# Kernel optimization log

Hardware: AMD Instinct MI355X
Metric: run time of the kernel (lower is better)

Reference implementation:

```python
import jax, jax.numpy as jnp
import numpy as np

NOPEN = 64
NNIN = 16
NUM_OUTPUT = 64
NLAYER = 4
H = 0.1
TF = 1.0
N_NODES = 50000
N_EDGES = 1600000


def setup_inputs() -> dict:
    key = jax.random.key(0)
    k1, k2, k3, k4, k5, k6 = jax.random.split(key, 6)
    xn = jax.random.normal(k1, (1, NNIN, N_NODES), dtype=jnp.float32)
    iInd = jax.random.randint(k2, (N_EDGES,), 0, N_NODES)
    jInd = jax.random.randint(k3, (N_EDGES,), 0, N_NODES)
    # learned parameters per original init
    K1Nopen = jax.random.normal(k4, (NOPEN, NNIN), dtype=jnp.float32) * 0.01
    KN1 = jnp.eye(NOPEN, dtype=jnp.float32) + jax.random.uniform(k5, (NOPEN, NOPEN), dtype=jnp.float32) * 0.001
    KNclose = jax.random.normal(k6, (NUM_OUTPUT, NOPEN), dtype=jnp.float32) * 0.01
    return {"xn": xn, "iInd": iInd, "jInd": jInd, "n_nodes": N_NODES,
            "K1Nopen": K1Nopen, "KN1": KN1, "KNclose": KNclose}


def _gcn_norm(I, J, n_nodes, dtype):
    # add self-loops, symmetric normalization deg^{-1/2}[row]*deg^{-1/2}[col]
    loops = jnp.arange(n_nodes, dtype=I.dtype)
    I2 = jnp.concatenate([I, loops])
    J2 = jnp.concatenate([J, loops])
    ew = jnp.ones(I2.shape[0], dtype=dtype)
    deg = jax.ops.segment_sum(ew, J2, num_segments=n_nodes)
    dinv = jnp.where(deg > 0, 1.0 / jnp.sqrt(deg), 0.0)
    w = dinv[I2] * dinv[J2]
    return I2, J2, w


def reference(xn, iInd, jInd, n_nodes, K1Nopen, KN1, KNclose):
    I, J, w = _gcn_norm(iInd, jInd, n_nodes, xn.dtype)  # [E+N]

    # OpenFlatLayer: 1x1 conv1d with K1Nopen + relu (openclose=True, norm=False)
    x = jax.nn.relu(jnp.einsum('oi,bin->bon', K1Nopen, xn))  # [1, nopen, N]

    dt = TF / NLAYER
    wb = w[None, None, :]
    for _ in range(NLAYER):
        # nodeGrad: edge features [1, nopen, E]
        g = wb * (x[:, :, I] - x[:, :, J])
        # singleLayer (openclose=False): conv(K), relu, conv(K.t())
        z = jax.nn.relu(jnp.einsum('oi,bie->boe', KN1, g))
        z = jnp.einsum('io,bie->boe', KN1, z)
        # edgeDiv: scatter-add w*z at I minus at J
        wz = jnp.moveaxis(wb * z, -1, 0)  # [E, 1, nopen]
        div = (jax.ops.segment_sum(wz, I, num_segments=n_nodes)
               - jax.ops.segment_sum(wz, J, num_segments=n_nodes))
        div = jnp.moveaxis(div, 0, -1)  # [1, nopen, N]
        # forward Euler: step layer returns -h*div, integrated with dt
        x = x - dt * H * div

    # CloseLayer: 1x1 conv1d, squeeze().t(), log_softmax over channels
    xc = jnp.einsum('oi,bin->bon', KNclose, x)[0].T  # [N, num_output]
    return jax.nn.log_softmax(xc, axis=1)
```

## Files before the change

### kernel.cpp

```cpp
#include <hip/hip_runtime.h>

#define NN 50000
#define NE 1600000
#define C 64
#define NIN 16
#define DTH 0.025f
#define ASC 16.0f
#define USC 64.0f
#define SDIV 16384.0f
#define SLOT 128

#define NB2 256
#define NPB 196
#define CAP 16384
#define ABLK 1024
#define EPB 1563
#define RND 2048
#define BINC 32
#define GSTR 16

typedef _Float16 f16x2 __attribute__((ext_vector_type(2)));
typedef float f32x2 __attribute__((ext_vector_type(2)));
union U32H2 { uint32_t u; f16x2 h; };

#define RL(x, l) __int_as_float(__builtin_amdgcn_readlane(__float_as_int(x), (l)))

__global__ void k_setup(const float* __restrict__ KN1, const float* __restrict__ KNc,
                        float* __restrict__ M2s, float* __restrict__ KMs,
                        int* __restrict__ gcur) {
    if (threadIdx.x < NB2) gcur[threadIdx.x * GSTR] = 0;
    for (int idx = threadIdx.x; idx < C * C; idx += blockDim.x) {
        int p = idx >> 6, o = idx & 63;
        float s1 = 0.f, s2 = 0.f;
        for (int i = 0; i < C; i++) {
            s1 = fmaf(KN1[o * C + i], KN1[p * C + i], s1);
            s2 = fmaf(KNc[o * C + i], KN1[p * C + i], s2);
        }
        M2s[idx] = s1;
        KMs[idx] = s2;
    }
}

static __device__ __forceinline__ void store_u8(uint32_t* __restrict__ u8, int n, int lane, float su) {
    float v1 = __shfl_down(su, 1, 64);
    float v2 = __shfl_down(su, 2, 64);
    float v3 = __shfl_down(su, 3, 64);
    if ((lane & 3) == 0) {
        int p0 = __builtin_amdgcn_cvt_pk_fp8_f32(su, v1, 0, false);
        int p1 = __builtin_amdgcn_cvt_pk_fp8_f32(v2, v3, p0, true);
        u8[n * 16 + (lane >> 2)] = (uint32_t)p1;
    }
}

__launch_bounds__(512)
__global__ void k_binA_open(const int* __restrict__ iInd, const int* __restrict__ jInd,
                            int* __restrict__ gcur, uint32_t* __restrict__ stg,
                            const float* __restrict__ xn, const float* __restrict__ K1,
                            const float* __restrict__ KN1, const float* __restrict__ KNc,
                            _Float16* __restrict__ u0, uint32_t* __restrict__ u8,
                            float* __restrict__ co) {
    __shared__ __align__(16) char smem[36864];
    __shared__ int bcnt[NB2];
    __shared__ int gbase[NB2];
    __shared__ float sxn[NIN][17];
    uint32_t (*bins)[BINC] = (uint32_t(*)[BINC])smem;
    int tid = threadIdx.x;
    int eBeg = blockIdx.x * EPB;
    int eEnd = eBeg + EPB; if (eEnd > NE) eEnd = NE;
    for (int rb = eBeg; rb < eEnd; rb += RND) {
        for (int b = tid; b < NB2; b += 512) bcnt[b] = 0;
        __syncthreads();
        int rEnd = rb + RND; if (rEnd > eEnd) rEnd = eEnd;
        for (int e = rb + tid; e < rEnd; e += 512) {
            int i = __builtin_nontemporal_load(&iInd[e]);
            int j = __builtin_nontemporal_load(&jInd[e]);
            {
                int b = (unsigned)i / NPB;
                uint32_t ent = ((unsigned)(i - b * NPB) << 17) | (unsigned)j;
                int pos = atomicAdd(&bcnt[b], 1);
                if (pos < BINC) bins[b][pos] = ent;
                else { int gp = atomicAdd(&gcur[b * GSTR], 1);
                       if (gp < CAP) stg[(size_t)b * CAP + gp] = ent; }
            }
            {
                int b = (unsigned)j / NPB;
                uint32_t ent = ((unsigned)(j - b * NPB) << 17) | 0x10000u | (unsigned)i;
                int pos = atomicAdd(&bcnt[b], 1);
                if (pos < BINC) bins[b][pos] = ent;
                else { int gp = atomicAdd(&gcur[b * GSTR], 1);
                       if (gp < CAP) stg[(size_t)b * CAP + gp] = ent; }
            }
        }
        __syncthreads();
        if (tid < NB2) {
            int c = bcnt[tid]; if (c > BINC) c = BINC;
            gbase[tid] = (c > 0) ? atomicAdd(&gcur[tid * GSTR], c) : 0;
        }
        __syncthreads();
        for (int idx = tid; idx < NB2 * BINC; idx += 512) {
            int b = idx >> 5, k = idx & (BINC - 1);
            int c = bcnt[b]; if (c > BINC) c = BINC;
            if (k < c) {
                int pos = gbase[b] + k;
                if (pos < CAP) stg[(size_t)b * CAP + pos] = bins[b][k];
            }
        }
        __syncthreads();
    }
    float* sK1 = (float*)smem;
    float* sU  = sK1 + NIN * C;
    float* sC  = sU + C * C;
    for (int idx = tid; idx < NIN * C; idx += 512) {
        int i = idx >> 6, o = idx & 63;
        sK1[idx] = K1[o * NIN + i];
    }
    for (int idx = tid; idx < C * C; idx += 512) {
        int o = idx >> 6, p = idx & 63;
        int sw = (o << 6) | (p ^ ((o & 7) << 2));
        sU[sw] = KN1[idx];
        sC[sw] = KNc[idx];
    }
    int wv = tid >> 6, lane = tid & 63;
    int mb = lane << 6, lx = (lane & 7) << 2;
    int w2 = wv * 2;
    int nit = 3 + (blockIdx.x < 53 ? 1 : 0);
    int fi = tid >> 4, ft = tid & 15;
    float vpre = 0.f;
    if (tid < 256) vpre = xn[fi * NN + blockIdx.x * 16 + ft];
    for (int it = 0; it < nit; it++) {
        __syncthreads();
        if (tid < 256) sxn[fi][ft] = vpre;
        __syncthreads();
        if (it + 1 < nit && tid < 256)
            vpre = xn[fi * NN + blockIdx.x * 16 + (it + 1) * 16384 + ft];
        int pr = blockIdx.x * 8 + wv + it * 8192;
        int nA = pr * 2, nB = nA + 1;
        float xA = 0.f, xB = 0.f;
#pragma unroll
        for (int i = 0; i < NIN; i++) {
            float k1 = sK1[i * C + lane];
            xA = fmaf(k1, sxn[i][w2], xA);
            xB = fmaf(k1, sxn[i][w2 + 1], xB);
        }
        xA = fmaxf(xA, 0.f); xB = fmaxf(xB, 0.f);
        float uA0 = 0.f, uA1 = 0.f, uB0 = 0.f, uB1 = 0.f;
        float cA0 = 0.f, cA1 = 0.f, cB0 = 0.f, cB1 = 0.f;
#pragma unroll
        for (int p0 = 0; p0 < C; p0 += 4) {
            const float4 mu = *(const float4*)&sU[mb + (p0 ^ lx)];
            const float4 mc = *(const float4*)&sC[mb + (p0 ^ lx)];
            float a0 = RL(xA, p0 + 0), a1 = RL(xA, p0 + 1);
            float a2 = RL(xA, p0 + 2), a3 = RL(xA, p0 + 3);
            float b0 = RL(xB, p0 + 0), b1 = RL(xB, p0 + 1);
            float b2 = RL(xB, p0 + 2), b3 = RL(xB, p0 + 3);
            uA0 = fmaf(mu.x, a0, uA0); uA1 = fmaf(mu.y, a1, uA1);
            uA0 = fmaf(mu.z, a2, uA0); uA1 = fmaf(mu.w, a3, uA1);
            uB0 = fmaf(mu.x, b0, uB0); uB1 = fmaf(mu.y, b1, uB1);
            uB0 = fmaf(mu.z, b2, uB0); uB1 = fmaf(mu.w, b3, uB1);
            cA0 = fmaf(mc.x, a0, cA0); cA1 = fmaf(mc.y, a1, cA1);
            cA0 = fmaf(mc.z, a2, cA0); cA1 = fmaf(mc.w, a3, cA1);
            cB0 = fmaf(mc.x, b0, cB0); cB1 = fmaf(mc.y, b1, cB1);
            cB0 = fmaf(mc.z, b2, cB0); cB1 = fmaf(mc.w, b3, cB1);
        }
        float uA = uA0 + uA1, uB = uB0 + uB1;
        u0[(size_t)nA * C + lane] = (_Float16)uA;
        u0[(size_t)nB * C + lane] = (_Float16)uB;
        store_u8(u8, nA, lane, uA * USC);
        store_u8(u8, nB, lane, uB * USC);
        co[(size_t)nA * C + lane] = cA0 + cA1;
        co[(size_t)nB * C + lane] = cB0 + cB1;
    }
}

#define LADJ (NPB * SLOT)
__launch_bounds__(1024)
__global__ void k_binB(const int* __restrict__ gcur, const uint32_t* __restrict__ stg,
                       unsigned* __restrict__ pk, float* __restrict__ dinv,
                       uint32_t* __restrict__ adjp) {
    __shared__ unsigned lcnt[NPB];
    __shared__ uint32_t ladj[LADJ];
    int b = blockIdx.x, tid = threadIdx.x;
    if (tid < NPB) lcnt[tid] = 0;
    __syncthreads();
    int cnt = gcur[b * GSTR]; if (cnt > CAP) cnt = CAP;
    int n0 = b * NPB;
    for (int k = tid; k < cnt; k += 1024) {
        uint32_t ent = stg[(size_t)b * CAP + k];
        int tl = (int)(ent >> 17);
        unsigned sign = (ent >> 16) & 1u;
        unsigned other = ent & 0xFFFFu;
        unsigned ret = atomicAdd(&lcnt[tl], 1u + (sign << 16));
        unsigned slot = ret & 0xFFFFu;
        if (slot < SLOT) ladj[(tl << 7) + slot] = other | (sign << 31);
    }
    __syncthreads();
    if (tid < NPB) {
        int n = n0 + tid;
        if (n < NN) {
            unsigned v = lcnt[tid];
            unsigned c = v & 0xFFFFu; if (c > SLOT) c = SLOT;
            unsigned deg = (v >> 16) + 1u;
            pk[n] = (deg << 16) | c;
            dinv[n] = 1.0f / sqrtf((float)deg);
        }
    }
    int nval = NN - n0; if (nval > NPB) nval = NPB; if (nval < 0) nval = 0;
    int totv = (nval << 7) >> 2;
    uint4* gdst = (uint4*)(adjp + ((size_t)n0 << 7));
    const uint4* lsrc = (const uint4*)ladj;
    for (int v = tid; v < totv; v += 1024) gdst[v] = lsrc[v];
}

__global__ void k_weight(const unsigned* __restrict__ pk, const float* __restrict__ dinv,
                         uint32_t* __restrict__ adjp) {
    int idx = blockIdx.x * 256 + threadIdx.x;
    int n = idx >> 7, p = idx & (SLOT - 1);
    int cnt = (int)(pk[n] & 0xFFFFu); if (cnt > SLOT) cnt = SLOT;
    int pad = (cnt + 31) & ~31;
    if (p < cnt) {
        uint32_t e = adjp[idx];
        int other = (int)(e & 0xFFFFu);
        float a = ASC * dinv[n] * dinv[other];
        if (e >> 31) a = -a;
        U32H2 t; t.u = (unsigned)other; t.h.y = (_Float16)a;
        adjp[idx] = t.u;
    } else if (p < pad) {
        adjp[idx] = 0u;
    }
}

#define ACCR(WW, QQ, A01, A23, U01, U23) {                                    \
    U32H2 aw; aw.u = (WW);                                                    \
    float a_ = (float)aw.h.y;                                                 \
    f32x2 av_; av_.x = a_; av_.y = a_;                                        \
    f32x2 lo_ = __builtin_amdgcn_cvt_pk_f32_fp8((int)(QQ), false);            \
    f32x2 hi_ = __builtin_amdgcn_cvt_pk_f32_fp8((int)(QQ), true);             \
    f32x2 t01_ = av_ * ((U01) - lo_);                                         \
    f32x2 t23_ = av_ * ((U23) - hi_);                                         \
    t01_ = __builtin_elementwise_max(t01_, zz);                               \
    t23_ = __builtin_elementwise_max(t23_, zz);                               \
    A01 = av_ * t01_ + A01;                                                   \
    A23 = av_ * t23_ + A23;                                                   \
}

#define GATHER2_BODY(PKA, ADJP, U8R)                                          \
    uint32_t unqA = (U8R)[nA * 16 + li];                                      \
    uint32_t unqB = (U8R)[nB * 16 + li];                                      \
    f32x2 uA01 = __builtin_amdgcn_cvt_pk_f32_fp8((int)unqA, false);           \
    f32x2 uA23 = __builtin_amdgcn_cvt_pk_f32_fp8((int)unqA, true);            \
    f32x2 uB01 = __builtin_amdgcn_cvt_pk_f32_fp8((int)unqB, false);           \
    f32x2 uB23 = __builtin_amdgcn_cvt_pk_f32_fp8((int)unqB, true);            \
    uint2 pk2_ = *(const uint2*)&(PKA)[nA];                                   \
    int degA = (int)(pk2_.x & 0xFFFFu); if (degA > SLOT) degA = SLOT;         \
    int degB = (int)(pk2_.y & 0xFFFFu); if (degB > SLOT) degB = SLOT;         \
    int padA = (degA + 31) & ~31, padB = (degB + 31) & ~31;                   \
    int baseA = nA << 7, baseB = nB << 7;                                     \
    int maxPad = padA > padB ? padA : padB;                                   \
    f32x2 zz; zz.x = 0.f; zz.y = 0.f;                                         \
    f32x2 aA01 = zz, aA23 = zz, aB01 = zz, aB23 = zz;                         \
    uint32_t wA[8], wB[8];                                                    \
    if (padA > 0) {                                                           \
        _Pragma("unroll")                                                     \
        for (int r = 0; r < 8; r++) wA[r] = (ADJP)[baseA + r * 4 + g];        \
    }                                                                         \
    if (padB > 0) {                                                           \
        _Pragma("unroll")                                                     \
        for (int r = 0; r < 8; r++) wB[r] = (ADJP)[baseB + r * 4 + g];        \
    }                                                                         \
    for (int c0 = 0; c0 < maxPad; c0 += 32) {                                 \
        uint32_t qA[8], qB[8], wA2[8], wB2[8];                                \
        bool dA = c0 < padA, dB = c0 < padB;                                  \
        bool dA2 = c0 + 32 < padA, dB2 = c0 + 32 < padB;                      \
        if (dA) {                                                             \
            _Pragma("unroll")                                                 \
            for (int r = 0; r < 8; r++) qA[r] = (U8R)[(wA[r] & 0xFFFFu) * 16 + li]; \
        }                                                                     \
        if (dB) {                                                             \
            _Pragma("unroll")                                                 \
            for (int r = 0; r < 8; r++) qB[r] = (U8R)[(wB[r] & 0xFFFFu) * 16 + li]; \
        }                                                                     \
        if (dA2) {                                                            \
            _Pragma("unroll")                                                 \
            for (int r = 0; r < 8; r++) wA2[r] = (ADJP)[baseA + c0 + 32 + r * 4 + g]; \
        }                                                                     \
        if (dB2) {                                                            \
            _Pragma("unroll")                                                 \
            for (int r = 0; r < 8; r++) wB2[r] = (ADJP)[baseB + c0 + 32 + r * 4 + g]; \
        }                                                                     \
        if (dA) {                                                             \
            _Pragma("unroll")                                                 \
            for (int r = 0; r < 8; r++) ACCR(wA[r], qA[r], aA01, aA23, uA01, uA23) \
        }                                                                     \
        if (dB) {                                                             \
            _Pragma("unroll")                                                 \
            for (int r = 0; r < 8; r++) ACCR(wB[r], qB[r], aB01, aB23, uB01, uB23) \
        }                                                                     \
        if (dA2) {                                                            \
            _Pragma("unroll")                                                 \
            for (int r = 0; r < 8; r++) wA[r] = wA2[r];                       \
        }                                                                     \
        if (dB2) {                                                            \
            _Pragma("unroll")                                                 \
            for (int r = 0; r < 8; r++) wB[r] = wB2[r];                       \
        }                                                                     \
    }                                                                         \
    float aA0 = aA01.x, aA1 = aA01.y, aA2 = aA23.x, aA3 = aA23.y;             \
    float aB0 = aB01.x, aB1 = aB01.y, aB2 = aB23.x, aB3 = aB23.y;             \
    aA0 += __shfl_xor(aA0, 16, 64); aA0 += __shfl_xor(aA0, 32, 64);           \
    aA1 += __shfl_xor(aA1, 16, 64); aA1 += __shfl_xor(aA1, 32, 64);           \
    aA2 += __shfl_xor(aA2, 16, 64); aA2 += __shfl_xor(aA2, 32, 64);           \
    aA3 += __shfl_xor(aA3, 16, 64); aA3 += __shfl_xor(aA3, 32, 64);           \
    aB0 += __shfl_xor(aB0, 16, 64); aB0 += __shfl_xor(aB0, 32, 64);           \
    aB1 += __shfl_xor(aB1, 16, 64); aB1 += __shfl_xor(aB1, 32, 64);           \
    aB2 += __shfl_xor(aB2, 16, 64); aB2 += __shfl_xor(aB2, 32, 64);           \
    aB3 += __shfl_xor(aB3, 16, 64); aB3 += __shfl_xor(aB3, 32, 64);           \
    float rA0 = __shfl(aA0, lane >> 2, 64), rA1 = __shfl(aA1, lane >> 2, 64); \
    float rA2 = __shfl(aA2, lane >> 2, 64), rA3 = __shfl(aA3, lane >> 2, 64); \
    float rB0 = __shfl(aB0, lane >> 2, 64), rB1 = __shfl(aB1, lane >> 2, 64); \
    float rB2 = __shfl(aB2, lane >> 2, 64), rB3 = __shfl(aB3, lane >> 2, 64); \
    float sA_lane = (lane & 2) ? ((lane & 1) ? rA3 : rA2)                     \
                               : ((lane & 1) ? rA1 : rA0);                    \
    float sB_lane = (lane & 2) ? ((lane & 1) ? rB3 : rB2)                     \
                               : ((lane & 1) ? rB1 : rB0);

#define STAGE_MT(SMT, SRC) {                                                  \
    for (int idx = threadIdx.x; idx < C * C; idx += 256) {                    \
        int p_ = idx >> 6, c_ = idx & 63;                                     \
        (SMT)[(c_ << 6) | (p_ ^ ((c_ & 7) << 2))] = (SRC)[idx];               \
    }                                                                         \
}

#define MATVEC2(SMT, SAV, SBV, DUA, DUB) {                                    \
    float mA0_ = 0.f, mA1_ = 0.f, mB0_ = 0.f, mB1_ = 0.f;                     \
    int mb_ = (lane << 6), lx_ = (lane & 7) << 2;                             \
    _Pragma("unroll")                                                         \
    for (int p0 = 0; p0 < 64; p0 += 4) {                                      \
        const float4 mv = *(const float4*)&(SMT)[mb_ + (p0 ^ lx_)];           \
        mA0_ = fmaf(mv.x, RL(SAV, p0 + 0), mA0_);                             \
        mA1_ = fmaf(mv.y, RL(SAV, p0 + 1), mA1_);                             \
        mA0_ = fmaf(mv.z, RL(SAV, p0 + 2), mA0_);                             \
        mA1_ = fmaf(mv.w, RL(SAV, p0 + 3), mA1_);                             \
        mB0_ = fmaf(mv.x, RL(SBV, p0 + 0), mB0_);                             \
        mB1_ = fmaf(mv.y, RL(SBV, p0 + 1), mB1_);                             \
        mB0_ = fmaf(mv.z, RL(SBV, p0 + 2), mB0_);                             \
        mB1_ = fmaf(mv.w, RL(SBV, p0 + 3), mB1_);                             \
    }                                                                         \
    DUA = mA0_ + mA1_; DUB = mB0_ + mB1_;                                     \
}

__launch_bounds__(256, 6)
__global__ void k_gather_upd(const unsigned* __restrict__ pk, const uint32_t* __restrict__ adjp,
                             const uint32_t* __restrict__ u8r, const _Float16* __restrict__ ucur,
                             const float* __restrict__ M2s, float* __restrict__ sacc,
                             _Float16* __restrict__ unext, uint32_t* __restrict__ u8w, int beta) {
    __shared__ float sMt[C * C];
    STAGE_MT(sMt, M2s)
    __syncthreads();
    int wv = threadIdx.x >> 6, lane = threadIdx.x & 63;
    int g = lane >> 4, li = lane & 15;
    int nA = (blockIdx.x * 4 + wv) * 2;
    int nB = nA + 1;
    GATHER2_BODY(pk, adjp, u8r)
    float duA, duB;
    MATVEC2(sMt, sA_lane, sB_lane, duA, duB)
    float unewA = (float)ucur[(size_t)nA * C + lane] - (DTH / SDIV) * duA;
    float unewB = (float)ucur[(size_t)nB * C + lane] - (DTH / SDIV) * duB;
    unext[(size_t)nA * C + lane] = (_Float16)unewA;
    unext[(size_t)nB * C + lane] = (_Float16)unewB;
    store_u8(u8w, nA, lane, unewA * USC);
    store_u8(u8w, nB, lane, unewB * USC);
    size_t ixA = (size_t)nA * C + lane, ixB = (size_t)nB * C + lane;
    sacc[ixA] = beta ? (sacc[ixA] + sA_lane) : sA_lane;
    sacc[ixB] = beta ? (sacc[ixB] + sB_lane) : sB_lane;
}

__launch_bounds__(256, 6)
__global__ void k_gather_close(const unsigned* __restrict__ pk, const uint32_t* __restrict__ adjp,
                               const uint32_t* __restrict__ u8r, const float* __restrict__ KMs,
                               const float* __restrict__ sacc, const float* __restrict__ co,
                               float* __restrict__ out) {
    __shared__ float sKMt[C * C];
    STAGE_MT(sKMt, KMs)
    __syncthreads();
    int wv = threadIdx.x >> 6, lane = threadIdx.x & 63;
    int g = lane >> 4, li = lane & 15;
    int nA = (blockIdx.x * 4 + wv) * 2;
    int nB = nA + 1;
    GATHER2_BODY(pk, adjp, u8r)
    float stotA = sA_lane + sacc[(size_t)nA * C + lane];
    float stotB = sB_lane + sacc[(size_t)nB * C + lane];
    float dxA, dxB;
    MATVEC2(sKMt, stotA, stotB, dxA, dxB)
    float oA = co[(size_t)nA * C + lane] - (DTH / SDIV) * dxA;
    float oB = co[(size_t)nB * C + lane] - (DTH / SDIV) * dxB;
    float mA = oA, mB = oB;
#pragma unroll
    for (int off2 = 32; off2; off2 >>= 1) {
        mA = fmaxf(mA, __shfl_xor(mA, off2, 64));
        mB = fmaxf(mB, __shfl_xor(mB, off2, 64));
    }
    float sumA = expf(oA - mA), sumB = expf(oB - mB);
#pragma unroll
    for (int off2 = 32; off2; off2 >>= 1) {
        sumA += __shfl_xor(sumA, off2, 64);
        sumB += __shfl_xor(sumB, off2, 64);
    }
    out[(size_t)nA * C + lane] = oA - mA - logf(sumA);
    out[(size_t)nB * C + lane] = oB - mB - logf(sumB);
}

extern "C" void kernel_launch(void* const* d_in, const int* in_sizes, int n_in,
                              void* d_out, int out_size, void* d_ws, size_t ws_size,
                              hipStream_t stream) {
    (void)in_sizes; (void)n_in; (void)out_size; (void)ws_size;
    const float* xn   = (const float*)d_in[0];
    const int* iInd   = (const int*)d_in[1];
    const int* jInd   = (const int*)d_in[2];
    const float* K1   = (const float*)d_in[4];
    const float* KN1  = (const float*)d_in[5];
    const float* KNc  = (const float*)d_in[6];
    float* out = (float*)d_out;

    char* base = (char*)d_ws;
    size_t off = 0;
    auto alloc = [&](size_t bytes) { char* p = base + off; off = (off + bytes + 255) & ~(size_t)255; return p; };
    float* M2s  = (float*)alloc(C * C * 4);
    float* KMs  = (float*)alloc(C * C * 4);
    int* gcur   = (int*)alloc(NB2 * GSTR * 4);
    unsigned* pk = (unsigned*)alloc(NN * 4);
    float* dinv = (float*)alloc(NN * 4);
    float* co   = (float*)alloc((size_t)NN * C * 4);
    float* sacc = (float*)alloc((size_t)NN * C * 4);
    _Float16* ua = (_Float16*)alloc((size_t)NN * C * 2);
    _Float16* ub = (_Float16*)alloc((size_t)NN * C * 2);
    uint32_t* u8a = (uint32_t*)alloc((size_t)NN * 16 * 4);
    uint32_t* u8b = (uint32_t*)alloc((size_t)NN * 16 * 4);
    uint32_t* stg = (uint32_t*)alloc((size_t)NB2 * CAP * 4);
    uint32_t* adjp = (uint32_t*)alloc((size_t)NN * SLOT * 4);

    k_setup<<<1, 256, 0, stream>>>(KN1, KNc, M2s, KMs, gcur);
    k_binA_open<<<ABLK, 512, 0, stream>>>(iInd, jInd, gcur, stg, xn, K1, KN1, KNc, ua, u8a, co);
    k_binB<<<NB2, 1024, 0, stream>>>(gcur, stg, pk, dinv, adjp);
    k_weight<<<(NN * SLOT) / 256, 256, 0, stream>>>(pk, dinv, adjp);

    const int GB = NN / 8;
    k_gather_upd<<<GB, 256, 0, stream>>>(pk, adjp, u8a, ua, M2s, sacc, ub, u8b, 0);
    k_gather_upd<<<GB, 256, 0, stream>>>(pk, adjp, u8b, ub, M2s, sacc, ua, u8a, 1);
    k_gather_upd<<<GB, 256, 0, stream>>>(pk, adjp, u8a, ua, M2s, sacc, ub, u8b, 1);
    k_gather_close<<<GB, 256, 0, stream>>>(pk, adjp, u8b, KMs, sacc, co, out);
}
```

Measured before the change: 460.7 us.

## Vectorize edge weighting, drop adjacency prefetch, use persistent gather grid

The edge-weight kernel now handles four adjacency slots per thread with 128-bit loads and stores, using a quarter of the threads. The gather loop no longer double-buffers the next chunk of adjacency words, which frees registers, and the launch bounds rise from 6 to 8 waves per SIMD. The gather and close kernels become grid-stride loops over a fixed 2048-block grid, so the 64x64 matrix is staged into shared memory once per block instead of once per 8 nodes. In exchange, adjacency loads are no longer overlapped with the feature gathers, which can expose more memory latency.

```diff
diff --git a/kernel.cpp b/kernel.cpp
--- a/kernel.cpp
+++ b/kernel.cpp
@@ -18,6 +18,7 @@
 #define RND 2048
 #define BINC 32
 #define GSTR 16
+#define GGRID 2048
 
 typedef _Float16 f16x2 __attribute__((ext_vector_type(2)));
 typedef float f32x2 __attribute__((ext_vector_type(2)));
@@ -211,22 +212,36 @@
     for (int v = tid; v < totv; v += 1024) gdst[v] = lsrc[v];
 }
 
+__launch_bounds__(256)
 __global__ void k_weight(const unsigned* __restrict__ pk, const float* __restrict__ dinv,
                          uint32_t* __restrict__ adjp) {
     int idx = blockIdx.x * 256 + threadIdx.x;
-    int n = idx >> 7, p = idx & (SLOT - 1);
+    int n = idx >> 5, p4 = (idx & 31) << 2;
     int cnt = (int)(pk[n] & 0xFFFFu); if (cnt > SLOT) cnt = SLOT;
     int pad = (cnt + 31) & ~31;
-    if (p < cnt) {
-        uint32_t e = adjp[idx];
-        int other = (int)(e & 0xFFFFu);
-        float a = ASC * dinv[n] * dinv[other];
-        if (e >> 31) a = -a;
-        U32H2 t; t.u = (unsigned)other; t.h.y = (_Float16)a;
-        adjp[idx] = t.u;
-    } else if (p < pad) {
-        adjp[idx] = 0u;
-    }
+    if (p4 >= pad) return;
+    size_t base = ((size_t)n << 7) + p4;
+    uint4 e = *(const uint4*)&adjp[base];
+    float dn = ASC * dinv[n];
+    uint4 o;
+    {
+        uint32_t r[4] = {e.x, e.y, e.z, e.w};
+        uint32_t w[4];
+#pragma unroll
+        for (int k = 0; k < 4; k++) {
+            if (p4 + k < cnt) {
+                int other = (int)(r[k] & 0xFFFFu);
+                float a = dn * dinv[other];
+                if (r[k] >> 31) a = -a;
+                U32H2 t; t.u = (unsigned)other; t.h.y = (_Float16)a;
+                w[k] = t.u;
+            } else {
+                w[k] = 0u;
+            }
+        }
+        o.x = w[0]; o.y = w[1]; o.z = w[2]; o.w = w[3];
+    }
+    *(uint4*)&adjp[base] = o;
 }
 
 #define ACCR(WW, QQ, A01, A23, U01, U23) {                                    \
@@ -258,35 +273,25 @@
     int maxPad = padA > padB ? padA : padB;                                   \
     f32x2 zz; zz.x = 0.f; zz.y = 0.f;                                         \
     f32x2 aA01 = zz, aA23 = zz, aB01 = zz, aB23 = zz;                         \
-    uint32_t wA[8], wB[8];                                                    \
-    if (padA > 0) {                                                           \
-        _Pragma("unroll")                                                     \
-        for (int r = 0; r < 8; r++) wA[r] = (ADJP)[baseA + r * 4 + g];        \
-    }                                                                         \
-    if (padB > 0) {                                                           \
-        _Pragma("unroll")                                                     \
-        for (int r = 0; r < 8; r++) wB[r] = (ADJP)[baseB + r * 4 + g];        \
-    }                                                                         \
     for (int c0 = 0; c0 < maxPad; c0 += 32) {                                 \
-        uint32_t qA[8], qB[8], wA2[8], wB2[8];                                \
+        uint32_t wA[8], qA[8], wB[8], qB[8];                                  \
         bool dA = c0 < padA, dB = c0 < padB;                                  \
-        bool dA2 = c0 + 32 < padA, dB2 = c0 + 32 < padB;                      \
         if (dA) {                                                             \
             _Pragma("unroll")                                                 \
+            for (int r = 0; r < 8; r++) wA[r] = (ADJP)[baseA + c0 + r * 4 + g]; \
+        }                                                                     \
+        if (dB) {                                                             \
+            _Pragma("unroll")                                                 \
+            for (int r = 0; r < 8; r++) wB[r] = (ADJP)[baseB + c0 + r * 4 + g]; \
+        }                                                                     \
+        if (dA) {                                                             \
+            _Pragma("unroll")                                                 \
             for (int r = 0; r < 8; r++) qA[r] = (U8R)[(wA[r] & 0xFFFFu) * 16 + li]; \
         }                                                                     \
         if (dB) {                                                             \
             _Pragma("unroll")                                                 \
             for (int r = 0; r < 8; r++) qB[r] = (U8R)[(wB[r] & 0xFFFFu) * 16 + li]; \
         }                                                                     \
-        if (dA2) {                                                            \
-            _Pragma("unroll")                                                 \
-            for (int r = 0; r < 8; r++) wA2[r] = (ADJP)[baseA + c0 + 32 + r * 4 + g]; \
-        }                                                                     \
-        if (dB2) {                                                            \
-            _Pragma("unroll")                                                 \
-            for (int r = 0; r < 8; r++) wB2[r] = (ADJP)[baseB + c0 + 32 + r * 4 + g]; \
-        }                                                                     \
         if (dA) {                                                             \
             _Pragma("unroll")                                                 \
             for (int r = 0; r < 8; r++) ACCR(wA[r], qA[r], aA01, aA23, uA01, uA23) \
@@ -294,14 +299,6 @@
         if (dB) {                                                             \
             _Pragma("unroll")                                                 \
             for (int r = 0; r < 8; r++) ACCR(wB[r], qB[r], aB01, aB23, uB01, uB23) \
-        }                                                                     \
-        if (dA2) {                                                            \
-            _Pragma("unroll")                                                 \
-            for (int r = 0; r < 8; r++) wA[r] = wA2[r];                       \
-        }                                                                     \
-        if (dB2) {                                                            \
-            _Pragma("unroll")                                                 \
-            for (int r = 0; r < 8; r++) wB[r] = wB2[r];                       \
         }                                                                     \
     }                                                                         \
     float aA0 = aA01.x, aA1 = aA01.y, aA2 = aA23.x, aA3 = aA23.y;             \
@@ -348,7 +345,7 @@
     DUA = mA0_ + mA1_; DUB = mB0_ + mB1_;                                     \
 }
 
-__launch_bounds__(256, 6)
+__launch_bounds__(256, 8)
 __global__ void k_gather_upd(const unsigned* __restrict__ pk, const uint32_t* __restrict__ adjp,
                              const uint32_t* __restrict__ u8r, const _Float16* __restrict__ ucur,
                              const float* __restrict__ M2s, float* __restrict__ sacc,
@@ -358,23 +355,25 @@
     __syncthreads();
     int wv = threadIdx.x >> 6, lane = threadIdx.x & 63;
     int g = lane >> 4, li = lane & 15;
-    int nA = (blockIdx.x * 4 + wv) * 2;
-    int nB = nA + 1;
-    GATHER2_BODY(pk, adjp, u8r)
-    float duA, duB;
-    MATVEC2(sMt, sA_lane, sB_lane, duA, duB)
-    float unewA = (float)ucur[(size_t)nA * C + lane] - (DTH / SDIV) * duA;
-    float unewB = (float)ucur[(size_t)nB * C + lane] - (DTH / SDIV) * duB;
-    unext[(size_t)nA * C + lane] = (_Float16)unewA;
-    unext[(size_t)nB * C + lane] = (_Float16)unewB;
-    store_u8(u8w, nA, lane, unewA * USC);
-    store_u8(u8w, nB, lane, unewB * USC);
-    size_t ixA = (size_t)nA * C + lane, ixB = (size_t)nB * C + lane;
-    sacc[ixA] = beta ? (sacc[ixA] + sA_lane) : sA_lane;
-    sacc[ixB] = beta ? (sacc[ixB] + sB_lane) : sB_lane;
-}
-
-__launch_bounds__(256, 6)
+    for (int grp = blockIdx.x; grp < NN / 8; grp += GGRID) {
+        int nA = (grp * 4 + wv) * 2;
+        int nB = nA + 1;
+        GATHER2_BODY(pk, adjp, u8r)
+        float duA, duB;
+        MATVEC2(sMt, sA_lane, sB_lane, duA, duB)
+        float unewA = (float)ucur[(size_t)nA * C + lane] - (DTH / SDIV) * duA;
+        float unewB = (float)ucur[(size_t)nB * C + lane] - (DTH / SDIV) * duB;
+        unext[(size_t)nA * C + lane] = (_Float16)unewA;
+        unext[(size_t)nB * C + lane] = (_Float16)unewB;
+        store_u8(u8w, nA, lane, unewA * USC);
+        store_u8(u8w, nB, lane, unewB * USC);
+        size_t ixA = (size_t)nA * C + lane, ixB = (size_t)nB * C + lane;
+        sacc[ixA] = beta ? (sacc[ixA] + sA_lane) : sA_lane;
+        sacc[ixB] = beta ? (sacc[ixB] + sB_lane) : sB_lane;
+    }
+}
+
+__launch_bounds__(256, 8)
 __global__ void k_gather_close(const unsigned* __restrict__ pk, const uint32_t* __restrict__ adjp,
                                const uint32_t* __restrict__ u8r, const float* __restrict__ KMs,
                                const float* __restrict__ sacc, const float* __restrict__ co,
@@ -384,29 +383,31 @@
     __syncthreads();
     int wv = threadIdx.x >> 6, lane = threadIdx.x & 63;
     int g = lane >> 4, li = lane & 15;
-    int nA = (blockIdx.x * 4 + wv) * 2;
-    int nB = nA + 1;
-    GATHER2_BODY(pk, adjp, u8r)
-    float stotA = sA_lane + sacc[(size_t)nA * C + lane];
-    float stotB = sB_lane + sacc[(size_t)nB * C + lane];
-    float dxA, dxB;
-    MATVEC2(sKMt, stotA, stotB, dxA, dxB)
-    float oA = co[(size_t)nA * C + lane] - (DTH / SDIV) * dxA;
-    float oB = co[(size_t)nB * C + lane] - (DTH / SDIV) * dxB;
-    float mA = oA, mB = oB;
+    for (int grp = blockIdx.x; grp < NN / 8; grp += GGRID) {
+        int nA = (grp * 4 + wv) * 2;
+        int nB = nA + 1;
+        GATHER2_BODY(pk, adjp, u8r)
+        float stotA = sA_lane + sacc[(size_t)nA * C + lane];
+        float stotB = sB_lane + sacc[(size_t)nB * C + lane];
+        float dxA, dxB;
+        MATVEC2(sKMt, stotA, stotB, dxA, dxB)
+        float oA = co[(size_t)nA * C + lane] - (DTH / SDIV) * dxA;
+        float oB = co[(size_t)nB * C + lane] - (DTH / SDIV) * dxB;
+        float mA = oA, mB = oB;
 #pragma unroll
-    for (int off2 = 32; off2; off2 >>= 1) {
-        mA = fmaxf(mA, __shfl_xor(mA, off2, 64));
-        mB = fmaxf(mB, __shfl_xor(mB, off2, 64));
-    }
-    float sumA = expf(oA - mA), sumB = expf(oB - mB);
+        for (int off2 = 32; off2; off2 >>= 1) {
+            mA = fmaxf(mA, __shfl_xor(mA, off2, 64));
+            mB = fmaxf(mB, __shfl_xor(mB, off2, 64));
+        }
+        float sumA = expf(oA - mA), sumB = expf(oB - mB);
 #pragma unroll
-    for (int off2 = 32; off2; off2 >>= 1) {
-        sumA += __shfl_xor(sumA, off2, 64);
-        sumB += __shfl_xor(sumB, off2, 64);
-    }
-    out[(size_t)nA * C + lane] = oA - mA - logf(sumA);
-    out[(size_t)nB * C + lane] = oB - mB - logf(sumB);
+        for (int off2 = 32; off2; off2 >>= 1) {
+            sumA += __shfl_xor(sumA, off2, 64);
+            sumB += __shfl_xor(sumB, off2, 64);
+        }
+        out[(size_t)nA * C + lane] = oA - mA - logf(sumA);
+        out[(size_t)nB * C + lane] = oB - mB - logf(sumB);
+    }
 }
 
 extern "C" void kernel_launch(void* const* d_in, const int* in_sizes, int n_in,
@@ -441,11 +442,10 @@
     k_setup<<<1, 256, 0, stream>>>(KN1, KNc, M2s, KMs, gcur);
     k_binA_open<<<ABLK, 512, 0, stream>>>(iInd, jInd, gcur, stg, xn, K1, KN1, KNc, ua, u8a, co);
     k_binB<<<NB2, 1024, 0, stream>>>(gcur, stg, pk, dinv, adjp);
-    k_weight<<<(NN * SLOT) / 256, 256, 0, stream>>>(pk, dinv, adjp);
-
-    const int GB = NN / 8;
-    k_gather_upd<<<GB, 256, 0, stream>>>(pk, adjp, u8a, ua, M2s, sacc, ub, u8b, 0);
-    k_gather_upd<<<GB, 256, 0, stream>>>(pk, adjp, u8b, ub, M2s, sacc, ua, u8a, 1);
-    k_gather_upd<<<GB, 256, 0, stream>>>(pk, adjp, u8a, ua, M2s, sacc, ub, u8b, 1);
-    k_gather_close<<<GB, 256, 0, stream>>>(pk, adjp, u8b, KMs, sacc, co, out);
-}
+    k_weight<<<(NN * SLOT / 4) / 256, 256, 0, stream>>>(pk, dinv, adjp);
+
+    k_gather_upd<<<GGRID, 256, 0, stream>>>(pk, adjp, u8a, ua, M2s, sacc, ub, u8b, 0);
+    k_gather_upd<<<GGRID, 256, 0, stream>>>(pk, adjp, u8b, ub, M2s, sacc, ua, u8a, 1);
+    k_gather_upd<<<GGRID, 256, 0, stream>>>(pk, adjp, u8a, ua, M2s, sacc, ub, u8b, 1);
+    k_gather_close<<<GGRID, 256, 0, stream>>>(pk, adjp, u8b, KMs, sacc, co, out);
+}
```

Measured after the change: 1.015 ms. +120.2%, slower.
